# Performance work log

Hardware: AMD Instinct MI355X
Metric: run time of the kernel (lower is better)

The kernel has to match this reference:

```python
import jax, jax.numpy as jnp
import numpy as np

# Dimensions: N sites, B batch, D bond dim, d physical dim, C output classes
N, B, D, d, C = 1024, 256, 16, 2, 10
STDDEV = 1e-5
INIT_DIAG = 1.0


def setup_inputs() -> dict:
    key = jax.random.key(0)
    k1, k2, k3 = jax.random.split(key, 3)
    x = jax.random.normal(k1, (N, B, d), dtype=jnp.float32)
    eye = jnp.eye(D, dtype=jnp.float32)
    # tensor[n,:,:,i] = init_diag * I + stddev * noise  (matches TF init)
    tensor = INIT_DIAG * eye[None, :, :, None] + STDDEV * jax.random.normal(k2, (N, D, D, d), dtype=jnp.float32)
    # Aout[c] = I + stddev * noise
    Aout = eye[None, :, :] + STDDEV * jax.random.normal(k3, (C, D, D), dtype=jnp.float32)
    return {"x": x, "tensor": tensor, "Aout": Aout}


def _chain_prod(A):
    # A: (n, b, D, D) -> ordered matrix-chain product (b, D, D), log-depth tree.
    # Faithful to parallel_contract: pairwise einsum per level; odd leftover is
    # kept at the end of the list (order-preserving, associativity-equivalent).
    while A.shape[0] > 1:
        n = A.shape[0]
        half = n // 2
        prod = jnp.einsum('nblk,nbkr->nblr', A[0:2 * half:2], A[1:2 * half:2])
        if n % 2 == 1:
            prod = jnp.concatenate([prod, A[-1:]], axis=0)
        A = prod
    return A[0]


def reference(x, tensor, Aout):
    # A: (N, B, D, D) site matrices after contracting input features
    A = jnp.einsum('nbi,nlri->nblr', x, tensor)
    nhalf = A.shape[0] // 2
    # Left half product, take row 0 (left boundary); right half, take col 0
    Al = _chain_prod(A[:nhalf])[:, 0, :]   # (B, D)
    Ar = _chain_prod(A[nhalf:])[:, :, 0]   # (B, D)
    # out[b,o] = Al[b] @ Aout[o] @ Ar[b]
    return jnp.einsum('bl,olr,br->bo', Al, Aout, Ar)
```

## Files before the change

kernel.cpp:

```cpp
#include <hip/hip_runtime.h>


#define BATCH  256
#define NCLS   10
#define NSITES 1024
#define NGRP   16
#define SEGLEN 16
#define NB     8

typedef __attribute__((ext_vector_type(4))) float f32x4;
typedef __attribute__((ext_vector_type(2))) float f32x2;
typedef __attribute__((ext_vector_type(4))) short short4b;
typedef __attribute__((ext_vector_type(2))) unsigned uint2v;
typedef __attribute__((ext_vector_type(4))) unsigned short us4;
typedef __attribute__((ext_vector_type(8))) short short8;

static __device__ __forceinline__ unsigned short bf16tr(float f) {
    return (unsigned short)(__builtin_bit_cast(unsigned, f) >> 16);
}
static __device__ __forceinline__ float bf16tof(unsigned short h) {
    return __builtin_bit_cast(float, (unsigned)h << 16);
}
static __device__ __forceinline__ unsigned fbits(float f) {
    return __builtin_bit_cast(unsigned, f);
}
static __device__ __forceinline__ unsigned pkhi(float hi, float lo) {
    return __builtin_amdgcn_perm(fbits(hi), fbits(lo), 0x07060302u);
}
static __device__ __forceinline__ short4b mk4(unsigned lo, unsigned hi) {
    uint2v u; u.x = lo; u.y = hi;
    return __builtin_bit_cast(short4b, u);
}
static __device__ __forceinline__ f32x4 mfma16(short4b a, short4b b, f32x4 c) {
#if __has_builtin(__builtin_amdgcn_mfma_f32_16x16x16bf16_1k)
    return __builtin_amdgcn_mfma_f32_16x16x16bf16_1k(a, b, c, 0, 0, 0);
#else
    f32x4 d;
    asm volatile("v_mfma_f32_16x16x16_bf16 %0, %1, %2, %3"
                 : "=v"(d) : "v"(a), "v"(b), "v"(c));
    return d;
#endif
}

__global__ __launch_bounds__(256) void chain_kernel(
    const float* __restrict__ x,
    const float* __restrict__ tensor,
    unsigned short* __restrict__ M2)
{
    __shared__ __align__(16) unsigned short rm[32 * 256];
    __shared__ __align__(16) unsigned short cm[32 * 256];
    const int t = threadIdx.x, wave = t >> 6, lane = t & 63;
    const int quad = lane >> 4, l15 = lane & 15;
    const int bt = blockIdx.x & 31, g = blockIdx.x >> 5;
    const int b0 = bt * NB;
    const int seg = g * 4 + wave, n0 = seg * SEGLEN;

    f32x4 d[NB];
#pragma unroll
    for (int j = 0; j < NB; ++j)
#pragma unroll
        for (int r = 0; r < 4; ++r) d[j][r] = (quad * 4 + r == l15) ? 1.0f : 0.0f;

    const float* __restrict__ tb =
        tensor + (size_t)n0 * 512 + ((size_t)(4 * quad) * 16 + l15) * 2;

#pragma unroll 4
    for (int s = 0; s < SEGLEN; ++s) {
        const int n = n0 + s;
        const float* __restrict__ ts = tb + (size_t)s * 512;
        const f32x2 v0 = __builtin_bit_cast(f32x2, *(const float2*)(ts));
        const f32x2 v1 = __builtin_bit_cast(f32x2, *(const float2*)(ts + 32));
        const f32x2 v2 = __builtin_bit_cast(f32x2, *(const float2*)(ts + 64));
        const f32x2 v3 = __builtin_bit_cast(f32x2, *(const float2*)(ts + 96));
        const float2* __restrict__ xp =
            (const float2*)(x + ((size_t)n * BATCH + b0) * 2);
        float2 xj[NB];
#pragma unroll
        for (int j = 0; j < NB; ++j) xj[j] = xp[j];
#pragma unroll
        for (int j = 0; j < NB; ++j) {
            const f32x2 xv = {xj[j].x, xj[j].y};
            const f32x2 p0 = v0 * xv;
            const f32x2 p1 = v1 * xv;
            const f32x2 p2 = v2 * xv;
            const f32x2 p3 = v3 * xv;
            const float a0 = p0[0] + p0[1];
            const float a1 = p1[0] + p1[1];
            const float a2 = p2[0] + p2[1];
            const float a3 = p3[0] + p3[1];
            const short4b af = mk4(pkhi(a1, a0), pkhi(a3, a2));
            const short4b wb = mk4(pkhi(d[j][1], d[j][0]), pkhi(d[j][3], d[j][2]));
            f32x4 c0 = {0.0f, 0.0f, 0.0f, 0.0f};
            d[j] = mfma16(af, wb, c0);
        }
    }

    if (wave & 1) {
#pragma unroll
        for (int j = 0; j < NB; ++j) {
            const int sl = j * 4 + wave;
#pragma unroll
            for (int r = 0; r < 4; ++r)
                rm[sl * 256 + (quad * 4 + r) * 16 + l15] = bf16tr(d[j][r]);
        }
    } else {
#pragma unroll
        for (int j = 0; j < NB; ++j) {
            const int sl = j * 4 + wave;
            us4 pk = {bf16tr(d[j][0]), bf16tr(d[j][1]), bf16tr(d[j][2]), bf16tr(d[j][3])};
            *(us4*)(cm + sl * 256 + l15 * 16 + quad * 4) = pk;
        }
    }
    __syncthreads();

    short4b af1v[4], bf1v[4];
#pragma unroll
    for (int i = 0; i < 4; ++i) {
        const int p = 4 * wave + i, j = p >> 1, h = p & 1;
        af1v[i] = __builtin_bit_cast(short4b,
            *(const uint2v*)(rm + (j * 4 + 2 * h + 1) * 256 + l15 * 16 + quad * 4));
        bf1v[i] = __builtin_bit_cast(short4b,
            *(const uint2v*)(cm + (j * 4 + 2 * h) * 256 + l15 * 16 + quad * 4));
    }
    __syncthreads();
#pragma unroll
    for (int i = 0; i < 4; ++i) {
        const int p = 4 * wave + i, j = p >> 1, h = p & 1;
        f32x4 c0 = {0.0f, 0.0f, 0.0f, 0.0f};
        f32x4 q = mfma16(af1v[i], bf1v[i], c0);
        const int sl = j * 4 + h;
        if (h) {
#pragma unroll
            for (int r = 0; r < 4; ++r)
                rm[sl * 256 + (quad * 4 + r) * 16 + l15] = bf16tr(q[r]);
        } else {
            us4 pk = {bf16tr(q[0]), bf16tr(q[1]), bf16tr(q[2]), bf16tr(q[3])};
            *(us4*)(cm + sl * 256 + l15 * 16 + quad * 4) = pk;
        }
    }
    __syncthreads();

#pragma unroll
    for (int i = 0; i < 2; ++i) {
        const int j = 2 * wave + i;
        const short4b af2 = __builtin_bit_cast(short4b,
            *(const uint2v*)(rm + (j * 4 + 1) * 256 + l15 * 16 + quad * 4));
        const short4b bf2 = __builtin_bit_cast(short4b,
            *(const uint2v*)(cm + (j * 4 + 0) * 256 + l15 * 16 + quad * 4));
        f32x4 c0 = {0.0f, 0.0f, 0.0f, 0.0f};
        f32x4 rr = mfma16(af2, bf2, c0);
        us4 pk = {bf16tr(rr[0]), bf16tr(rr[1]), bf16tr(rr[2]), bf16tr(rr[3])};
        *(us4*)(M2 + ((size_t)(b0 + j) * NGRP + g) * 256 + l15 * 16 + quad * 4) = pk;
    }
}

__global__ __launch_bounds__(256) void combine_kernel(
    const unsigned short* __restrict__ M2,
    const float* __restrict__ Aout,
    float* __restrict__ out)
{
    __shared__ __align__(16) unsigned short rm[16 * 256];
    __shared__ __align__(16) unsigned short cm[16 * 256];
    const int b = blockIdx.x, t = threadIdx.x;
    const int wave = t >> 6, lane = t & 63, quad = lane >> 4, l15 = lane & 15;

    const short8* __restrict__ src = (const short8*)(M2 + (size_t)b * NGRP * 256);
#pragma unroll
    for (int i2 = 0; i2 < 2; ++i2) {
        const int i = t + 256 * i2;
        const short8 v = src[i];
        *((short8*)cm + i) = v;
        const int mat = i >> 5, c = (i >> 1) & 15, r0 = (i & 1) * 8;
#pragma unroll
        for (int e = 0; e < 8; ++e)
            rm[mat * 256 + (r0 + e) * 16 + c] = (unsigned short)v[e];
    }
    __syncthreads();

    for (int lvl = 0; lvl < 3; ++lvl) {
        const int np = 8 >> lvl;
        short4b afr[2], bfr[2];
        int pids[2], nmine = 0;
        for (int p = wave; p < np; p += 4) {
            afr[nmine] = __builtin_bit_cast(short4b,
                 *(const uint2v*)(rm + (2 * p + 1) * 256 + l15 * 16 + quad * 4));
            bfr[nmine] = __builtin_bit_cast(short4b,
                 *(const uint2v*)(cm + (2 * p) * 256 + l15 * 16 + quad * 4));
            pids[nmine] = p; ++nmine;
        }
        __syncthreads();
        for (int ii = 0; ii < nmine; ++ii) {
            f32x4 c0 = {0.0f, 0.0f, 0.0f, 0.0f};
            f32x4 r = mfma16(afr[ii], bfr[ii], c0);
            const int p = pids[ii];
#pragma unroll
            for (int rr = 0; rr < 4; ++rr)
                rm[p * 256 + (quad * 4 + rr) * 16 + l15] = bf16tr(r[rr]);
            us4 pk = {bf16tr(r[0]), bf16tr(r[1]), bf16tr(r[2]), bf16tr(r[3])};
            *(us4*)(cm + p * 256 + l15 * 16 + quad * 4) = pk;
        }
        __syncthreads();
    }

    if (t < NCLS * 16) {
        const int o = t >> 4, r = t & 15;
        const float vr = bf16tof(rm[256 + r]);
        float s = 0.0f;
#pragma unroll
        for (int l = 0; l < 16; ++l)
            s = __builtin_fmaf(bf16tof(rm[l * 16]), Aout[((size_t)o * 16 + l) * 16 + r], s);
        s *= vr;
#pragma unroll
        for (int off = 8; off > 0; off >>= 1)
            s += __shfl_xor(s, off, 16);
        if (r == 0) out[(size_t)b * NCLS + o] = s;
    }
}

extern "C" void kernel_launch(void* const* d_in, const int* in_sizes, int n_in,
                              void* d_out, int out_size, void* d_ws, size_t ws_size,
                              hipStream_t stream)
{
    const float* x      = (const float*)d_in[0];
    const float* tensor = (const float*)d_in[1];
    const float* Aout   = (const float*)d_in[2];
    float* out = (float*)d_out;

    unsigned short* M2 = (unsigned short*)d_ws;

    chain_kernel<<<BATCH * NGRP / NB, 256, 0, stream>>>(x, tensor, M2);
    combine_kernel<<<BATCH, 256, 0, stream>>>(M2, Aout, out);
}
```

Before: 76.18 us.

## Halve segment length and use 8-wave blocks with an extra in-block reduction level

After: 75.63 us. No clear change (-0.7%).

```diff
diff --git a/kernel.cpp b/kernel.cpp
--- a/kernel.cpp
+++ b/kernel.cpp
@@ -5,7 +5,7 @@
 #define NCLS   10
 #define NSITES 1024
 #define NGRP   16
-#define SEGLEN 16
+#define SEGLEN 8
 #define NB     8
 
 typedef __attribute__((ext_vector_type(4))) float f32x4;
@@ -42,18 +42,17 @@
 #endif
 }
 
-__global__ __launch_bounds__(256) void chain_kernel(
+__global__ __launch_bounds__(512, 4) void chain_kernel(
     const float* __restrict__ x,
     const float* __restrict__ tensor,
     unsigned short* __restrict__ M2)
 {
-    __shared__ __align__(16) unsigned short rm[32 * 256];
-    __shared__ __align__(16) unsigned short cm[32 * 256];
-    const int t = threadIdx.x, wave = t >> 6, lane = t & 63;
+    __shared__ __align__(16) unsigned short stg[64 * 256];
+    const int t = threadIdx.x, w = t >> 6, lane = t & 63;
     const int quad = lane >> 4, l15 = lane & 15;
-    const int bt = blockIdx.x & 31, g = blockIdx.x >> 5;
+    const int bt = blockIdx.x & 31, o = blockIdx.x >> 5;
     const int b0 = bt * NB;
-    const int seg = g * 4 + wave, n0 = seg * SEGLEN;
+    const int seg = o * 8 + w, n0 = seg * SEGLEN;
 
     f32x4 d[NB];
 #pragma unroll
@@ -95,20 +94,20 @@
         }
     }
 
-    if (wave & 1) {
+    if (w & 1) {
 #pragma unroll
         for (int j = 0; j < NB; ++j) {
-            const int sl = j * 4 + wave;
+            const int sl = j * 8 + w;
 #pragma unroll
             for (int r = 0; r < 4; ++r)
-                rm[sl * 256 + (quad * 4 + r) * 16 + l15] = bf16tr(d[j][r]);
+                stg[sl * 256 + (quad * 4 + r) * 16 + l15] = bf16tr(d[j][r]);
         }
     } else {
 #pragma unroll
         for (int j = 0; j < NB; ++j) {
-            const int sl = j * 4 + wave;
+            const int sl = j * 8 + w;
             us4 pk = {bf16tr(d[j][0]), bf16tr(d[j][1]), bf16tr(d[j][2]), bf16tr(d[j][3])};
-            *(us4*)(cm + sl * 256 + l15 * 16 + quad * 4) = pk;
+            *(us4*)(stg + sl * 256 + l15 * 16 + quad * 4) = pk;
         }
     }
     __syncthreads();
@@ -116,41 +115,67 @@
     short4b af1v[4], bf1v[4];
 #pragma unroll
     for (int i = 0; i < 4; ++i) {
-        const int p = 4 * wave + i, j = p >> 1, h = p & 1;
+        const int p = 4 * w + i, j = p >> 2, h = p & 3;
         af1v[i] = __builtin_bit_cast(short4b,
-            *(const uint2v*)(rm + (j * 4 + 2 * h + 1) * 256 + l15 * 16 + quad * 4));
+            *(const uint2v*)(stg + (j * 8 + 2 * h + 1) * 256 + l15 * 16 + quad * 4));
         bf1v[i] = __builtin_bit_cast(short4b,
-            *(const uint2v*)(cm + (j * 4 + 2 * h) * 256 + l15 * 16 + quad * 4));
+            *(const uint2v*)(stg + (j * 8 + 2 * h) * 256 + l15 * 16 + quad * 4));
     }
     __syncthreads();
 #pragma unroll
     for (int i = 0; i < 4; ++i) {
-        const int p = 4 * wave + i, j = p >> 1, h = p & 1;
+        const int p = 4 * w + i, j = p >> 2, h = p & 3;
         f32x4 c0 = {0.0f, 0.0f, 0.0f, 0.0f};
         f32x4 q = mfma16(af1v[i], bf1v[i], c0);
-        const int sl = j * 4 + h;
-        if (h) {
+        const int sl = j * 8 + h;
+        if (h & 1) {
 #pragma unroll
             for (int r = 0; r < 4; ++r)
-                rm[sl * 256 + (quad * 4 + r) * 16 + l15] = bf16tr(q[r]);
+                stg[sl * 256 + (quad * 4 + r) * 16 + l15] = bf16tr(q[r]);
         } else {
             us4 pk = {bf16tr(q[0]), bf16tr(q[1]), bf16tr(q[2]), bf16tr(q[3])};
-            *(us4*)(cm + sl * 256 + l15 * 16 + quad * 4) = pk;
-        }
-    }
-    __syncthreads();
-
+            *(us4*)(stg + sl * 256 + l15 * 16 + quad * 4) = pk;
+        }
+    }
+    __syncthreads();
+
+    short4b af2v[2], bf2v[2];
 #pragma unroll
     for (int i = 0; i < 2; ++i) {
-        const int j = 2 * wave + i;
-        const short4b af2 = __builtin_bit_cast(short4b,
-            *(const uint2v*)(rm + (j * 4 + 1) * 256 + l15 * 16 + quad * 4));
-        const short4b bf2 = __builtin_bit_cast(short4b,
-            *(const uint2v*)(cm + (j * 4 + 0) * 256 + l15 * 16 + quad * 4));
+        const int p = 2 * w + i, j = p >> 1, k = p & 1;
+        af2v[i] = __builtin_bit_cast(short4b,
+            *(const uint2v*)(stg + (j * 8 + 2 * k + 1) * 256 + l15 * 16 + quad * 4));
+        bf2v[i] = __builtin_bit_cast(short4b,
+            *(const uint2v*)(stg + (j * 8 + 2 * k) * 256 + l15 * 16 + quad * 4));
+    }
+    __syncthreads();
+#pragma unroll
+    for (int i = 0; i < 2; ++i) {
+        const int p = 2 * w + i, j = p >> 1, k = p & 1;
         f32x4 c0 = {0.0f, 0.0f, 0.0f, 0.0f};
-        f32x4 rr = mfma16(af2, bf2, c0);
+        f32x4 r = mfma16(af2v[i], bf2v[i], c0);
+        const int sl = j * 8 + k;
+        if (k) {
+#pragma unroll
+            for (int rr = 0; rr < 4; ++rr)
+                stg[sl * 256 + (quad * 4 + rr) * 16 + l15] = bf16tr(r[rr]);
+        } else {
+            us4 pk = {bf16tr(r[0]), bf16tr(r[1]), bf16tr(r[2]), bf16tr(r[3])};
+            *(us4*)(stg + sl * 256 + l15 * 16 + quad * 4) = pk;
+        }
+    }
+    __syncthreads();
+
+    {
+        const int j = w;
+        const short4b af3 = __builtin_bit_cast(short4b,
+            *(const uint2v*)(stg + (j * 8 + 1) * 256 + l15 * 16 + quad * 4));
+        const short4b bf3 = __builtin_bit_cast(short4b,
+            *(const uint2v*)(stg + (j * 8 + 0) * 256 + l15 * 16 + quad * 4));
+        f32x4 c0 = {0.0f, 0.0f, 0.0f, 0.0f};
+        f32x4 rr = mfma16(af3, bf3, c0);
         us4 pk = {bf16tr(rr[0]), bf16tr(rr[1]), bf16tr(rr[2]), bf16tr(rr[3])};
-        *(us4*)(M2 + ((size_t)(b0 + j) * NGRP + g) * 256 + l15 * 16 + quad * 4) = pk;
+        *(us4*)(M2 + ((size_t)(b0 + j) * NGRP + o) * 256 + l15 * 16 + quad * 4) = pk;
     }
 }
 
@@ -228,6 +253,6 @@
 
     unsigned short* M2 = (unsigned short*)d_ws;
 
-    chain_kernel<<<BATCH * NGRP / NB, 256, 0, stream>>>(x, tensor, M2);
+    chain_kernel<<<(NSITES / (SEGLEN * 8)) * (BATCH / NB), 512, 0, stream>>>(x, tensor, M2);
     combine_kernel<<<BATCH, 256, 0, stream>>>(M2, Aout, out);
 }
```
